# Kernel tuning notes

Measured on AMD Instinct MI355X. Metric: run time of the kernel, lower is better.

## Reference

```python
import jax, jax.numpy as jnp
import numpy as np

N_NODES = 100000


def gcn_conv(x, edge_index, W, b):
    """PyG-style GCNConv: add self-loops, symmetric deg^{-1/2} normalization,
    then scatter-sum of transformed source features into targets."""
    n = x.shape[0]
    loops = jnp.arange(n, dtype=edge_index.dtype)
    row = jnp.concatenate([edge_index[0], loops])  # source
    col = jnp.concatenate([edge_index[1], loops])  # target
    deg = jax.ops.segment_sum(jnp.ones_like(col, dtype=x.dtype), col, num_segments=n)
    dinv = jnp.where(deg > 0, jax.lax.rsqrt(deg), 0.0)
    norm = dinv[row] * dinv[col]  # [E+N]
    h = x @ W  # [N, out]
    msg = h[row] * norm[:, None]  # gather + scale, [E+N, out]
    out = jax.ops.segment_sum(msg, col, num_segments=n)
    return out + b


def setup_inputs() -> dict:
    key = jax.random.key(0)
    k1, k2, k3, k4, k5 = jax.random.split(key, 5)
    x = jax.random.normal(k1, (N_NODES, 972), dtype=jnp.float32)
    edge_index = jax.random.randint(k2, (2, 1600000), 0, N_NODES, dtype=jnp.int64)
    edge_label_index = jax.random.randint(k3, (2, 1000000), 0, N_NODES, dtype=jnp.int64)
    W1 = jax.random.normal(k4, (384, 128), dtype=jnp.float32) * (1.0 / np.sqrt(384))
    b1 = jnp.zeros((128,), dtype=jnp.float32)
    W2 = jax.random.normal(k5, (128, 64), dtype=jnp.float32) * (1.0 / np.sqrt(128))
    b2 = jnp.zeros((64,), dtype=jnp.float32)
    return {"x": x, "edge_index": edge_index, "edge_label_index": edge_label_index,
            "W1": W1, "b1": b1, "W2": W2, "b2": b2}


def reference(x, edge_index, edge_label_index, W1, b1, W2, b2):
    # encode: slice features, two GCN layers with relu between
    h = x[:, 588:]  # [N, 384]
    h = jax.nn.relu(gcn_conv(h, edge_index, W1, b1))
    z = gcn_conv(h, edge_index, W2, b2)  # [N, 64]
    # decode: gather-dot-sum over labeled edges
    logits = jnp.sum(z[edge_label_index[0]] * z[edge_label_index[1]], axis=-1)
    return logits
```

## Files before the change

### kernel.cpp

```cpp
#include <hip/hip_runtime.h>
#include <hip/hip_bf16.h>

#define N_NODES 100000
#define N_EDGES 1600000
#define N_LBL   1000000
#define XC 972
#define XO 588
#define D1 128
#define D2 64
#define GEMM1_BLOCKS ((N_NODES + 63) / 64)
#define PLACE_BLOCKS (N_EDGES / 512)
#define MEGA_BLOCKS  (GEMM1_BLOCKS + PLACE_BLOCKS)

typedef float f32x4 __attribute__((ext_vector_type(4)));
typedef short bf16x8 __attribute__((ext_vector_type(8)));

__device__ inline unsigned f2bf(float f) {
    unsigned u = __float_as_uint(f);
    return (u + 0x7fffu + ((u >> 16) & 1u)) >> 16;
}
__device__ inline float bf_lo(unsigned v) { return __uint_as_float(v << 16); }
__device__ inline float bf_hi(unsigned v) { return __uint_as_float(v & 0xffff0000u); }

__device__ inline unsigned pack_bf2(float lo, float hi) {
    union { __hip_bfloat162 h; unsigned u; } p;
    p.h = __float22bfloat162_rn(make_float2(lo, hi));
    return p.u;
}
__device__ inline bf16x8 to_bf8(float4 a, float4 b) {
    union { __hip_bfloat162 h[4]; bf16x8 v; } u;
    u.h[0] = __float22bfloat162_rn(make_float2(a.x, a.y));
    u.h[1] = __float22bfloat162_rn(make_float2(a.z, a.w));
    u.h[2] = __float22bfloat162_rn(make_float2(b.x, b.y));
    u.h[3] = __float22bfloat162_rn(make_float2(b.z, b.w));
    return u.v;
}
__device__ inline void add8(float (&a)[8], uint4 u) {
    a[0] += bf_lo(u.x); a[1] += bf_hi(u.x);
    a[2] += bf_lo(u.y); a[3] += bf_hi(u.y);
    a[4] += bf_lo(u.z); a[5] += bf_hi(u.z);
    a[6] += bf_lo(u.w); a[7] += bf_hi(u.w);
}
__device__ inline void fma8(float (&a)[8], uint4 u, float s) {
    a[0] = fmaf(bf_lo(u.x), s, a[0]); a[1] = fmaf(bf_hi(u.x), s, a[1]);
    a[2] = fmaf(bf_lo(u.y), s, a[2]); a[3] = fmaf(bf_hi(u.y), s, a[3]);
    a[4] = fmaf(bf_lo(u.z), s, a[4]); a[5] = fmaf(bf_hi(u.z), s, a[5]);
    a[6] = fmaf(bf_lo(u.w), s, a[6]); a[7] = fmaf(bf_hi(u.w), s, a[7]);
}
__device__ inline float dot8(uint4 a, uint4 c) {
    return bf_lo(a.x) * bf_lo(c.x) + bf_hi(a.x) * bf_hi(c.x)
         + bf_lo(a.y) * bf_lo(c.y) + bf_hi(a.y) * bf_hi(c.y)
         + bf_lo(a.z) * bf_lo(c.z) + bf_hi(a.z) * bf_hi(c.z)
         + bf_lo(a.w) * bf_lo(c.w) + bf_hi(a.w) * bf_hi(c.w);
}

__global__ __launch_bounds__(256) void k_prep(const float* __restrict__ W1,
                                              const float* __restrict__ W2,
                                              unsigned short* __restrict__ w1p,
                                              unsigned short* __restrict__ w2p,
                                              unsigned* __restrict__ cursor) {
    int i = blockIdx.x * 256 + threadIdx.x;
    if (i < N_NODES) cursor[i] = 0u;
    if (i < 49152) {
        int j = i & 7, lane = (i >> 3) & 63, nt = (i >> 9) & 7, ks = i >> 12;
        int k = ks * 32 + ((lane >> 4) << 3) + j;
        int n = (nt << 4) + (lane & 15);
        w1p[i] = (unsigned short)f2bf(W1[k * D1 + n]);
    } else if (i < 57344) {
        int t = i - 49152;
        int j = t & 7, lane = (t >> 3) & 63, nt = (t >> 9) & 3, ks = t >> 11;
        int k = ks * 32 + ((lane >> 4) << 3) + j;
        int n = (nt << 4) + (lane & 15);
        w2p[t] = (unsigned short)f2bf(W2[k * D2 + n]);
    }
}

__global__ __launch_bounds__(256) void k_mega(const float* __restrict__ x,
                                              const unsigned short* __restrict__ w1p,
                                              unsigned short* __restrict__ s1,
                                              const int* __restrict__ erow,
                                              const int* __restrict__ ecol,
                                              unsigned* __restrict__ cursor,
                                              int* __restrict__ srcidx) {
    const int bid = blockIdx.x;
    const int g = bid / 3, r3 = bid % 3;
    if (r3 == 0) {
        const int lane = threadIdx.x & 63;
        const int wid  = threadIdx.x >> 6;
        const int lrow = lane & 15;
        const int kq   = lane >> 4;

        const int row0 = g * 64 + wid * 16;
        const int rc = min(row0 + lrow, N_NODES - 1);
        const float* pA = x + (size_t)rc * XC + XO + (kq << 3);

        f32x4 acc[8];
#pragma unroll
        for (int t = 0; t < 8; ++t) acc[t] = (f32x4)0.f;

#pragma unroll 2
        for (int ks = 0; ks < 12; ++ks) {
            float4 a0 = *reinterpret_cast<const float4*>(pA + ks * 32);
            float4 a1 = *reinterpret_cast<const float4*>(pA + ks * 32 + 4);
            bf16x8 aA = to_bf8(a0, a1);
#pragma unroll
            for (int t = 0; t < 8; ++t) {
                bf16x8 bf = *reinterpret_cast<const bf16x8*>(
                    w1p + ((size_t)((ks * 8 + t) * 64 + lane) << 3));
                acc[t] = __builtin_amdgcn_mfma_f32_16x16x32_bf16(aA, bf, acc[t], 0, 0, 0);
            }
        }

        const int rowq = row0 + kq * 4;
#pragma unroll
        for (int r = 0; r < 4; ++r) {
            int rw = rowq + r;
            if (rw < N_NODES) {
#pragma unroll
                for (int t = 0; t < 8; ++t)
                    s1[(size_t)rw * D1 + lrow + t * 16] =
                        (unsigned short)f2bf(acc[t][r]);
            }
        }
    } else {
        int pb = bid - g - 1;
        int pe = pb * 256 + threadIdx.x;
        int2 rw = *reinterpret_cast<const int2*>(erow + 2 * pe);
        int2 cl = *reinterpret_cast<const int2*>(ecol + 2 * pe);
        unsigned j0 = atomicAdd(&cursor[cl.x], 1u);
        srcidx[((size_t)cl.x << 6) + j0] = rw.x;
        unsigned j1 = atomicAdd(&cursor[cl.y], 1u);
        srcidx[((size_t)cl.y << 6) + j1] = rw.y;
    }
}

__global__ __launch_bounds__(256) void k_fused(const unsigned short* __restrict__ s1,
                                               const int* __restrict__ srcidx,
                                               const unsigned* __restrict__ deg,
                                               const float* __restrict__ b1,
                                               const unsigned short* __restrict__ w2p,
                                               unsigned short* __restrict__ s2) {
    const int lane = threadIdx.x & 63;
    const int wid  = threadIdx.x >> 6;
    const int n    = lane & 15;
    const int kq   = lane >> 4;
    const int base = blockIdx.x * 64 + wid * 16;
    const int c  = base + n;
    const int cc = min(c, N_NODES - 1);

    const int cnt = (int)deg[cc];
    const float dc = rsqrtf((float)(cnt + 1));

    float acc[4][8];
#pragma unroll
    for (int p = 0; p < 4; ++p)
#pragma unroll
        for (int j = 0; j < 8; ++j) acc[p][j] = 0.f;

    {
        const unsigned short* srow = s1 + (size_t)cc * D1 + (kq << 3);
        fma8(acc[0], *reinterpret_cast<const uint4*>(srow),      dc);
        fma8(acc[1], *reinterpret_cast<const uint4*>(srow + 32), dc);
        fma8(acc[2], *reinterpret_cast<const uint4*>(srow + 64), dc);
        fma8(acc[3], *reinterpret_cast<const uint4*>(srow + 96), dc);
    }

    const int* sp = srcidx + ((size_t)cc << 6);
    int j = 0;
    int4 idx;
    if (cnt >= 4) idx = *reinterpret_cast<const int4*>(sp);
    for (; j + 4 <= cnt; j += 4) {
        int4 cur = idx;
        if (j + 8 <= cnt) idx = *reinterpret_cast<const int4*>(sp + j + 4);
        const unsigned short* p0 = s1 + (size_t)cur.x * D1 + (kq << 3);
        const unsigned short* p1 = s1 + (size_t)cur.y * D1 + (kq << 3);
        const unsigned short* p2 = s1 + (size_t)cur.z * D1 + (kq << 3);
        const unsigned short* p3 = s1 + (size_t)cur.w * D1 + (kq << 3);
        unsigned g0 = deg[cur.x], g1 = deg[cur.y], g2 = deg[cur.z], g3 = deg[cur.w];
        uint4 a0 = *reinterpret_cast<const uint4*>(p0);
        uint4 a1 = *reinterpret_cast<const uint4*>(p0 + 32);
        uint4 a2 = *reinterpret_cast<const uint4*>(p0 + 64);
        uint4 a3 = *reinterpret_cast<const uint4*>(p0 + 96);
        uint4 b0 = *reinterpret_cast<const uint4*>(p1);
        uint4 b1x = *reinterpret_cast<const uint4*>(p1 + 32);
        uint4 b2 = *reinterpret_cast<const uint4*>(p1 + 64);
        uint4 b3 = *reinterpret_cast<const uint4*>(p1 + 96);
        uint4 c0 = *reinterpret_cast<const uint4*>(p2);
        uint4 c1 = *reinterpret_cast<const uint4*>(p2 + 32);
        uint4 c2 = *reinterpret_cast<const uint4*>(p2 + 64);
        uint4 c3 = *reinterpret_cast<const uint4*>(p2 + 96);
        uint4 e0 = *reinterpret_cast<const uint4*>(p3);
        uint4 e1 = *reinterpret_cast<const uint4*>(p3 + 32);
        uint4 e2 = *reinterpret_cast<const uint4*>(p3 + 64);
        uint4 e3 = *reinterpret_cast<const uint4*>(p3 + 96);
        float d0 = rsqrtf((float)(g0 + 1u));
        float d1 = rsqrtf((float)(g1 + 1u));
        float d2 = rsqrtf((float)(g2 + 1u));
        float d3 = rsqrtf((float)(g3 + 1u));
        fma8(acc[0], a0, d0); fma8(acc[1], a1, d0);
        fma8(acc[2], a2, d0); fma8(acc[3], a3, d0);
        fma8(acc[0], b0, d1); fma8(acc[1], b1x, d1);
        fma8(acc[2], b2, d1); fma8(acc[3], b3, d1);
        fma8(acc[0], c0, d2); fma8(acc[1], c1, d2);
        fma8(acc[2], c2, d2); fma8(acc[3], c3, d2);
        fma8(acc[0], e0, d3); fma8(acc[1], e1, d3);
        fma8(acc[2], e2, d3); fma8(acc[3], e3, d3);
    }
    for (; j < cnt; ++j) {
        int r = sp[j];
        float dr = rsqrtf((float)(deg[r] + 1u));
        const unsigned short* rr = s1 + (size_t)r * D1 + (kq << 3);
        fma8(acc[0], *reinterpret_cast<const uint4*>(rr),      dr);
        fma8(acc[1], *reinterpret_cast<const uint4*>(rr + 32), dr);
        fma8(acc[2], *reinterpret_cast<const uint4*>(rr + 64), dr);
        fma8(acc[3], *reinterpret_cast<const uint4*>(rr + 96), dr);
    }

    bf16x8 af[4];
#pragma unroll
    for (int p = 0; p < 4; ++p) {
        const float* bp = b1 + p * 32 + (kq << 3);
        float4 ba = *reinterpret_cast<const float4*>(bp);
        float4 bb = *reinterpret_cast<const float4*>(bp + 4);
        float4 h0 = make_float4(fmaxf(fmaf(acc[p][0], dc, ba.x), 0.f),
                                fmaxf(fmaf(acc[p][1], dc, ba.y), 0.f),
                                fmaxf(fmaf(acc[p][2], dc, ba.z), 0.f),
                                fmaxf(fmaf(acc[p][3], dc, ba.w), 0.f));
        float4 h1 = make_float4(fmaxf(fmaf(acc[p][4], dc, bb.x), 0.f),
                                fmaxf(fmaf(acc[p][5], dc, bb.y), 0.f),
                                fmaxf(fmaf(acc[p][6], dc, bb.z), 0.f),
                                fmaxf(fmaf(acc[p][7], dc, bb.w), 0.f));
        af[p] = to_bf8(h0, h1);
    }

    f32x4 acc2[4];
#pragma unroll
    for (int nt = 0; nt < 4; ++nt) acc2[nt] = (f32x4)0.f;
#pragma unroll
    for (int ks = 0; ks < 4; ++ks)
#pragma unroll
        for (int nt = 0; nt < 4; ++nt) {
            bf16x8 bf = *reinterpret_cast<const bf16x8*>(
                w2p + ((size_t)((ks * 4 + nt) * 64 + lane) << 3));
            acc2[nt] = __builtin_amdgcn_mfma_f32_16x16x32_bf16(af[ks], bf, acc2[nt], 0, 0, 0);
        }

#pragma unroll
    for (int r = 0; r < 4; ++r) {
        int rw = base + kq * 4 + r;
        if (rw < N_NODES) {
            float dm = rsqrtf((float)(deg[rw] + 1u));
#pragma unroll
            for (int nt = 0; nt < 4; ++nt)
                s2[(size_t)rw * D2 + nt * 16 + n] =
                    (unsigned short)f2bf(acc2[nt][r] * dm);
        }
    }
}

__global__ __launch_bounds__(256) void k_gather2(const unsigned short* __restrict__ s2,
                                                 const int* __restrict__ srcidx,
                                                 const unsigned* __restrict__ deg,
                                                 const float* __restrict__ b,
                                                 uint4* __restrict__ zv) {
    const int c    = blockIdx.x * 32 + (threadIdx.x >> 3);
    const int l8   = threadIdx.x & 7;

    float a[8];
#pragma unroll
    for (int j = 0; j < 8; ++j) a[j] = 0.f;
    add8(a, *reinterpret_cast<const uint4*>(s2 + (size_t)c * D2 + (l8 << 3)));

    const int cnt = (int)deg[c];
    const int* sp = srcidx + ((size_t)c << 6);
    int j = 0;
    for (; j + 8 <= cnt; j += 8) {
        int4 i0 = *reinterpret_cast<const int4*>(sp + j);
        int4 i1 = *reinterpret_cast<const int4*>(sp + j + 4);
        uint4 u0 = *reinterpret_cast<const uint4*>(s2 + (size_t)i0.x * D2 + (l8 << 3));
        uint4 u1 = *reinterpret_cast<const uint4*>(s2 + (size_t)i0.y * D2 + (l8 << 3));
        uint4 u2 = *reinterpret_cast<const uint4*>(s2 + (size_t)i0.z * D2 + (l8 << 3));
        uint4 u3 = *reinterpret_cast<const uint4*>(s2 + (size_t)i0.w * D2 + (l8 << 3));
        uint4 u4 = *reinterpret_cast<const uint4*>(s2 + (size_t)i1.x * D2 + (l8 << 3));
        uint4 u5 = *reinterpret_cast<const uint4*>(s2 + (size_t)i1.y * D2 + (l8 << 3));
        uint4 u6 = *reinterpret_cast<const uint4*>(s2 + (size_t)i1.z * D2 + (l8 << 3));
        uint4 u7 = *reinterpret_cast<const uint4*>(s2 + (size_t)i1.w * D2 + (l8 << 3));
        add8(a, u0); add8(a, u1); add8(a, u2); add8(a, u3);
        add8(a, u4); add8(a, u5); add8(a, u6); add8(a, u7);
    }
    for (; j + 4 <= cnt; j += 4) {
        int4 idx = *reinterpret_cast<const int4*>(sp + j);
        uint4 u0 = *reinterpret_cast<const uint4*>(s2 + (size_t)idx.x * D2 + (l8 << 3));
        uint4 u1 = *reinterpret_cast<const uint4*>(s2 + (size_t)idx.y * D2 + (l8 << 3));
        uint4 u2 = *reinterpret_cast<const uint4*>(s2 + (size_t)idx.z * D2 + (l8 << 3));
        uint4 u3 = *reinterpret_cast<const uint4*>(s2 + (size_t)idx.w * D2 + (l8 << 3));
        add8(a, u0); add8(a, u1); add8(a, u2); add8(a, u3);
    }
    for (; j < cnt; ++j) {
        int r = sp[j];
        add8(a, *reinterpret_cast<const uint4*>(s2 + (size_t)r * D2 + (l8 << 3)));
    }
    const float d = rsqrtf((float)(cnt + 1));
    const float4 b0 = reinterpret_cast<const float4*>(b)[l8 * 2];
    const float4 b1v = reinterpret_cast<const float4*>(b)[l8 * 2 + 1];
    uint4 o;
    o.x = pack_bf2(fmaf(a[0], d, b0.x),  fmaf(a[1], d, b0.y));
    o.y = pack_bf2(fmaf(a[2], d, b0.z),  fmaf(a[3], d, b0.w));
    o.z = pack_bf2(fmaf(a[4], d, b1v.x), fmaf(a[5], d, b1v.y));
    o.w = pack_bf2(fmaf(a[6], d, b1v.z), fmaf(a[7], d, b1v.w));
    zv[(size_t)c * 8 + l8] = o;
}

__global__ __launch_bounds__(256) void k_score(const uint4* __restrict__ Z,
                                               const int* __restrict__ ea,
                                               const int* __restrict__ eb,
                                               float* __restrict__ out) {
    int tid = blockIdx.x * 256 + threadIdx.x;
    int p = tid >> 3;
    int l = tid & 7;
    if (p >= N_LBL / 4) return;
    int4 us = *reinterpret_cast<const int4*>(ea + 4 * p);
    int4 vs = *reinterpret_cast<const int4*>(eb + 4 * p);
    uint4 a0 = Z[(size_t)us.x * 8 + l];
    uint4 c0 = Z[(size_t)vs.x * 8 + l];
    uint4 a1 = Z[(size_t)us.y * 8 + l];
    uint4 c1 = Z[(size_t)vs.y * 8 + l];
    uint4 a2 = Z[(size_t)us.z * 8 + l];
    uint4 c2 = Z[(size_t)vs.z * 8 + l];
    uint4 a3 = Z[(size_t)us.w * 8 + l];
    uint4 c3 = Z[(size_t)vs.w * 8 + l];
    float p0 = dot8(a0, c0);
    float p1 = dot8(a1, c1);
    float p2 = dot8(a2, c2);
    float p3 = dot8(a3, c3);
    p0 += __shfl_down(p0, 4, 8);  p1 += __shfl_down(p1, 4, 8);
    p2 += __shfl_down(p2, 4, 8);  p3 += __shfl_down(p3, 4, 8);
    p0 += __shfl_down(p0, 2, 8);  p1 += __shfl_down(p1, 2, 8);
    p2 += __shfl_down(p2, 2, 8);  p3 += __shfl_down(p3, 2, 8);
    p0 += __shfl_down(p0, 1, 8);  p1 += __shfl_down(p1, 1, 8);
    p2 += __shfl_down(p2, 1, 8);  p3 += __shfl_down(p3, 1, 8);
    if (l == 0)
        *reinterpret_cast<float4*>(out + 4 * p) = make_float4(p0, p1, p2, p3);
}

extern "C" void kernel_launch(void* const* d_in, const int* in_sizes, int n_in,
                              void* d_out, int out_size, void* d_ws, size_t ws_size,
                              hipStream_t stream) {
    const float* x   = (const float*)d_in[0];
    const int*   ei  = (const int*)d_in[1];
    const int*   eli = (const int*)d_in[2];
    const float* W1  = (const float*)d_in[3];
    const float* b1  = (const float*)d_in[4];
    const float* W2  = (const float*)d_in[5];
    const float* b2  = (const float*)d_in[6];
    float* out = (float*)d_out;

    char* ws = (char*)d_ws;
    unsigned*       cursor = (unsigned*)(ws + 0);
    unsigned short* w1p    = (unsigned short*)(ws + 400000);
    unsigned short* w2p    = (unsigned short*)(ws + 498304);
    int*            srcidx = (int*)(ws + 514688);
    unsigned short* s1     = (unsigned short*)(ws + 26114688);
    unsigned short* s2     = (unsigned short*)(ws + 51714688);
    unsigned short* z      = (unsigned short*)(ws + 64514688);

    k_prep   <<<392, 256, 0, stream>>>(W1, W2, w1p, w2p, cursor);
    k_mega   <<<MEGA_BLOCKS, 256, 0, stream>>>(x, w1p, s1, ei, ei + N_EDGES,
                                               cursor, srcidx);
    k_fused  <<<(N_NODES + 63) / 64, 256, 0, stream>>>(s1, srcidx, cursor, b1, w2p, s2);
    k_gather2<<<N_NODES / 32, 256, 0, stream>>>(s2, srcidx, cursor, b2, (uint4*)z);
    k_score  <<<(N_LBL / 4 * 8 + 255) / 256, 256, 0, stream>>>((const uint4*)z, eli,
                                                               eli + N_LBL, out);
}
```

Before: 290.9 us.

## Simplify work distribution: one edge per thread, two labels per group, no interleaving

Drops the interleaved GEMM/placement block schedule in the mega kernel, so all GEMM blocks run first and then placement blocks. Placement now handles one edge per thread, and the scoring kernel handles two label pairs per 8-lane group instead of four. This yields more, lighter threads, giving up per-thread memory-level parallelism and the overlap of compute-bound and atomic-bound blocks.

Result: faster. 270.4 us (-7.1%).

```diff
diff --git a/kernel.cpp b/kernel.cpp
--- a/kernel.cpp
+++ b/kernel.cpp
@@ -9,8 +9,7 @@
 #define D1 128
 #define D2 64
 #define GEMM1_BLOCKS ((N_NODES + 63) / 64)
-#define PLACE_BLOCKS (N_EDGES / 512)
-#define MEGA_BLOCKS  (GEMM1_BLOCKS + PLACE_BLOCKS)
+#define PLACE_BLOCKS (N_EDGES / 256)
 
 typedef float f32x4 __attribute__((ext_vector_type(4)));
 typedef short bf16x8 __attribute__((ext_vector_type(8)));
@@ -82,15 +81,13 @@
                                               const int* __restrict__ ecol,
                                               unsigned* __restrict__ cursor,
                                               int* __restrict__ srcidx) {
-    const int bid = blockIdx.x;
-    const int g = bid / 3, r3 = bid % 3;
-    if (r3 == 0) {
+    if (blockIdx.x < GEMM1_BLOCKS) {
         const int lane = threadIdx.x & 63;
         const int wid  = threadIdx.x >> 6;
         const int lrow = lane & 15;
         const int kq   = lane >> 4;
 
-        const int row0 = g * 64 + wid * 16;
+        const int row0 = blockIdx.x * 64 + wid * 16;
         const int rc = min(row0 + lrow, N_NODES - 1);
         const float* pA = x + (size_t)rc * XC + XO + (kq << 3);
 
@@ -123,14 +120,10 @@
             }
         }
     } else {
-        int pb = bid - g - 1;
-        int pe = pb * 256 + threadIdx.x;
-        int2 rw = *reinterpret_cast<const int2*>(erow + 2 * pe);
-        int2 cl = *reinterpret_cast<const int2*>(ecol + 2 * pe);
-        unsigned j0 = atomicAdd(&cursor[cl.x], 1u);
-        srcidx[((size_t)cl.x << 6) + j0] = rw.x;
-        unsigned j1 = atomicAdd(&cursor[cl.y], 1u);
-        srcidx[((size_t)cl.y << 6) + j1] = rw.y;
+        int e = (blockIdx.x - GEMM1_BLOCKS) * 256 + threadIdx.x;
+        int c = ecol[e];
+        unsigned j = atomicAdd(&cursor[c], 1u);
+        srcidx[((size_t)c << 6) + j] = erow[e];
     }
 }
 
@@ -318,29 +311,18 @@
     int tid = blockIdx.x * 256 + threadIdx.x;
     int p = tid >> 3;
     int l = tid & 7;
-    if (p >= N_LBL / 4) return;
-    int4 us = *reinterpret_cast<const int4*>(ea + 4 * p);
-    int4 vs = *reinterpret_cast<const int4*>(eb + 4 * p);
+    int2 us = *reinterpret_cast<const int2*>(ea + 2 * p);
+    int2 vs = *reinterpret_cast<const int2*>(eb + 2 * p);
     uint4 a0 = Z[(size_t)us.x * 8 + l];
     uint4 c0 = Z[(size_t)vs.x * 8 + l];
     uint4 a1 = Z[(size_t)us.y * 8 + l];
     uint4 c1 = Z[(size_t)vs.y * 8 + l];
-    uint4 a2 = Z[(size_t)us.z * 8 + l];
-    uint4 c2 = Z[(size_t)vs.z * 8 + l];
-    uint4 a3 = Z[(size_t)us.w * 8 + l];
-    uint4 c3 = Z[(size_t)vs.w * 8 + l];
     float p0 = dot8(a0, c0);
     float p1 = dot8(a1, c1);
-    float p2 = dot8(a2, c2);
-    float p3 = dot8(a3, c3);
     p0 += __shfl_down(p0, 4, 8);  p1 += __shfl_down(p1, 4, 8);
-    p2 += __shfl_down(p2, 4, 8);  p3 += __shfl_down(p3, 4, 8);
     p0 += __shfl_down(p0, 2, 8);  p1 += __shfl_down(p1, 2, 8);
-    p2 += __shfl_down(p2, 2, 8);  p3 += __shfl_down(p3, 2, 8);
     p0 += __shfl_down(p0, 1, 8);  p1 += __shfl_down(p1, 1, 8);
-    p2 += __shfl_down(p2, 1, 8);  p3 += __shfl_down(p3, 1, 8);
-    if (l == 0)
-        *reinterpret_cast<float4*>(out + 4 * p) = make_float4(p0, p1, p2, p3);
+    if (l == 0) *reinterpret_cast<float2*>(out + 2 * p) = make_float2(p0, p1);
 }
 
 extern "C" void kernel_launch(void* const* d_in, const int* in_sizes, int n_in,
@@ -365,10 +347,10 @@
     unsigned short* z      = (unsigned short*)(ws + 64514688);
 
     k_prep   <<<392, 256, 0, stream>>>(W1, W2, w1p, w2p, cursor);
-    k_mega   <<<MEGA_BLOCKS, 256, 0, stream>>>(x, w1p, s1, ei, ei + N_EDGES,
-                                               cursor, srcidx);
+    k_mega   <<<GEMM1_BLOCKS + PLACE_BLOCKS, 256, 0, stream>>>(x, w1p, s1, ei,
+                                                               ei + N_EDGES, cursor, srcidx);
     k_fused  <<<(N_NODES + 63) / 64, 256, 0, stream>>>(s1, srcidx, cursor, b1, w2p, s2);
     k_gather2<<<N_NODES / 32, 256, 0, stream>>>(s2, srcidx, cursor, b2, (uint4*)z);
-    k_score  <<<(N_LBL / 4 * 8 + 255) / 256, 256, 0, stream>>>((const uint4*)z, eli,
+    k_score  <<<(size_t)N_LBL * 8 / 2 / 256, 256, 0, stream>>>((const uint4*)z, eli,
                                                                eli + N_LBL, out);
 }
```
